# Kernel tuning notes

Measured on AMD Instinct MI355X. Metric: run time of the kernel, lower is better.

The kernel has to match this reference:

```python
import jax, jax.numpy as jnp
import numpy as np

ATTEN = 32  # window half-size; window = 2*ATTEN + 1


def _pos_enc(seq_len, hidden_size):
    # Faithful to original: pos_enc[pos, j] = pos / 10000**(2*(j//2)/hidden_size)
    # then sin on even columns, cos on odd columns. Shape [seq_len, seq_len].
    pos = jnp.arange(seq_len, dtype=jnp.float32)[:, None]
    j = jnp.arange(seq_len)
    inv = jnp.power(jnp.float32(10000.0), (2.0 * (j // 2).astype(jnp.float32)) / hidden_size)
    angle = pos / inv[None, :]
    return jnp.where((j % 2 == 0)[None, :], jnp.sin(angle), jnp.cos(angle))


def setup_inputs() -> dict:
    key = jax.random.key(0)
    ks = jax.random.split(key, 8)
    B, S, D_in, H, D_out = 4, 2048, 2048, 128, 2
    sd_in = 1.0 / np.sqrt(D_in)
    sd_h = 1.0 / np.sqrt(H)
    return {
        "x": jax.random.normal(ks[0], (B, S, D_in), dtype=jnp.float32),
        "W1": jax.random.normal(ks[1], (D_in, H), dtype=jnp.float32) * sd_in,
        "b1": jnp.zeros((H,), dtype=jnp.float32),
        "Wq": jax.random.normal(ks[2], (H, H), dtype=jnp.float32) * sd_h,
        "Wk": jax.random.normal(ks[3], (H, H), dtype=jnp.float32) * sd_h,
        "Wv": jax.random.normal(ks[4], (H, H), dtype=jnp.float32) * sd_h,
        "Wo": jax.random.normal(ks[5], (H, D_out), dtype=jnp.float32) * sd_h,
        "bo": jnp.zeros((D_out,), dtype=jnp.float32),
    }


def reference(x, W1, b1, Wq, Wk, Wv, Wo, bo):
    B, S, _ = x.shape
    H = W1.shape[1]
    scale = jnp.float32(np.sqrt(float(H)))

    x = x + _pos_enc(S, H)[None]                      # [B,S,D_in] (D_in == S)
    h = jax.nn.relu(x @ W1 + b1)                      # [B,S,H]

    # Replicate pad + roll(+wraparound) + stack + slice via a gather.
    # x_nei[b,i,j] = padded[b, (i + 2a - j) mod (S+2a)], j in [0, 2a].
    a = ATTEN
    L = S + 2 * a
    padded = jnp.pad(h, ((0, 0), (a, a), (0, 0)))     # [B,L,H]
    idx = (jnp.arange(S)[:, None] + 2 * a - jnp.arange(2 * a + 1)[None, :]) % L
    x_nei = padded[:, idx, :]                         # [B,S,2a+1,H]

    q = h @ Wq                                        # [B,S,H]
    k = x_nei @ Wk                                    # [B,S,2a+1,H]
    v = x_nei @ Wv                                    # [B,S,2a+1,H]

    scores = jnp.einsum('bid,bijd->bij', q, k) / scale
    atten_weights = jax.nn.softmax(scores, axis=-1)   # [B,S,2a+1]
    context = jnp.einsum('bij,bijd->bid', atten_weights, v) / scale  # extra /sqrt(H), faithful to source
    output = context @ Wo + bo                        # [B,S,D_out]
    return output, atten_weights
```

## Files before the change

### kernel.cpp

```cpp
#include <hip/hip_runtime.h>
#include <hip/hip_bf16.h>

typedef __attribute__((ext_vector_type(8))) _Float16 half8;
typedef __attribute__((ext_vector_type(4))) _Float16 half4;
typedef __attribute__((ext_vector_type(4))) float f32x4;

#define MFMAH(a,b,c) __builtin_amdgcn_mfma_f32_16x16x32_f16(a,b,c,0,0,0)

#define LOG2_10K_64 0.2076205059304595f
#define INV2PI 0.15915494309189535f

__global__ __launch_bounds__(256) void k_prep(const float* __restrict__ W1,
                                              const float* __restrict__ Wq,
                                              const float* __restrict__ Wk,
                                              const float* __restrict__ Wv,
                                              _Float16* __restrict__ W1t,
                                              _Float16* __restrict__ Wqkvt) {
  const int bid = blockIdx.x, tid = threadIdx.x;
  if (bid < 64) {
    __shared__ float Tl[64][65];
    const int kt0 = (bid >> 1) * 64, nt0 = (bid & 1) * 64;
    const int row = tid >> 2, c0 = (tid & 3) * 16;
#pragma unroll
    for (int e = 0; e < 16; e += 4) {
      float4 f = *(const float4*)(W1 + (size_t)(kt0 + row) * 128 + nt0 + c0 + e);
      Tl[row][c0 + e] = f.x; Tl[row][c0 + e + 1] = f.y;
      Tl[row][c0 + e + 2] = f.z; Tl[row][c0 + e + 3] = f.w;
    }
    __syncthreads();
    const int nrow = tid >> 2, kc0 = (tid & 3) * 16;
    _Float16* wp = W1t + (size_t)(nt0 + nrow) * 2048 + kt0 + kc0;
#pragma unroll
    for (int e = 0; e < 16; ++e) wp[e] = (_Float16)Tl[kc0 + e][nrow];
  } else {
    int r = (bid - 64) * 256 + tid;
    if (r < 3 * 16384) {
      int m = r >> 14, e = r & 16383;
      int n = e >> 7, k = e & 127;
      const float* W = (m == 0) ? Wq : (m == 1) ? Wk : Wv;
      Wqkvt[r] = (_Float16)W[k * 128 + n];
    }
  }
}

__global__ __launch_bounds__(512) void k_fused(const float* __restrict__ x,
                                               const _Float16* __restrict__ W1t,
                                               const _Float16* __restrict__ Wqkv,
                                               const float* __restrict__ b1,
                                               _Float16* __restrict__ Qg,
                                               _Float16* __restrict__ Kg,
                                               _Float16* __restrict__ Vg) {
  __shared__ _Float16 As[2][16][136];
  const int tid = threadIdx.x;
  const int lane = tid & 63, wv = tid >> 6;
  const int fr = lane & 15, kg8 = (lane >> 4) * 8;
  const int i0 = blockIdx.x * 16;
  const int arow = tid >> 5, akc = (tid & 31) * 4;
  const float sf = (float)((i0 + arow) & 2047);
  const float* xrow = x + (size_t)(i0 + arow) * 2048 + akc;
  const _Float16* wrow = W1t + (size_t)(wv * 16 + fr) * 2048 + kg8;

  auto loadB = [&](int s, half8* b) {
    const _Float16* p = wrow + s * 128;
#pragma unroll
    for (int kk = 0; kk < 4; ++kk) b[kk] = *(const half8*)(p + kk * 32);
  };
  auto stageA = [&](int buf, int s, float4 xa) {
    const int kb = s * 128 + akc;
    float c0 = exp2f((float)(kb >> 1) * -LOG2_10K_64) * INV2PI;
    float c1 = exp2f((float)((kb >> 1) + 1) * -LOG2_10K_64) * INV2PI;
    float r0 = __builtin_fmaf(sf, c0, -rintf(sf * c0));
    float r1 = __builtin_fmaf(sf, c1, -rintf(sf * c1));
    half4 av;
    av[0] = (_Float16)(xa.x + __builtin_amdgcn_sinf(r0));
    av[1] = (_Float16)(xa.y + __builtin_amdgcn_cosf(r0));
    av[2] = (_Float16)(xa.z + __builtin_amdgcn_sinf(r1));
    av[3] = (_Float16)(xa.w + __builtin_amdgcn_cosf(r1));
    *(half4*)&As[buf][arow][akc] = av;
  };

  float4 xaA = *(const float4*)(xrow);
  float4 xaB = *(const float4*)(xrow + 128);
  half8 bcur[4], bnxt[4];
  loadB(0, bcur);
  stageA(0, 0, xaA);
  __syncthreads();

  f32x4 acc = {};
#pragma unroll 1
  for (int i = 0; i < 7; ++i) {
    const int s = 2 * i;
    xaA = *(const float4*)(xrow + (s + 2) * 128);
    loadB(s + 1, bnxt);
#pragma unroll
    for (int kk = 0; kk < 4; ++kk) {
      half8 a = *(const half8*)&As[0][fr][kk * 32 + kg8];
      acc = MFMAH(a, bcur[kk], acc);
    }
    stageA(1, s + 1, xaB);
    __syncthreads();
    xaB = *(const float4*)(xrow + (s + 3) * 128);
    loadB(s + 2, bcur);
#pragma unroll
    for (int kk = 0; kk < 4; ++kk) {
      half8 a = *(const half8*)&As[1][fr][kk * 32 + kg8];
      acc = MFMAH(a, bnxt[kk], acc);
    }
    stageA(0, s + 2, xaA);
    __syncthreads();
  }
  loadB(15, bnxt);
#pragma unroll
  for (int kk = 0; kk < 4; ++kk) {
    half8 a = *(const half8*)&As[0][fr][kk * 32 + kg8];
    acc = MFMAH(a, bcur[kk], acc);
  }
  stageA(1, 15, xaB);
  __syncthreads();
#pragma unroll
  for (int kk = 0; kk < 4; ++kk) {
    half8 a = *(const half8*)&As[1][fr][kk * 32 + kg8];
    acc = MFMAH(a, bnxt[kk], acc);
  }
  __syncthreads();

  _Float16 (*Hs)[136] = As[0];
  {
    const int col = wv * 16 + fr;
    const float bv = b1[col];
#pragma unroll
    for (int r = 0; r < 4; ++r) {
      float v = acc[r] + bv;
      v = v > 0.f ? v : 0.f;
      Hs[(lane >> 4) * 4 + r][col] = (_Float16)v;
    }
  }
  __syncthreads();
  const _Float16* wqrow = Wqkv + (size_t)(wv * 16 + fr) * 128 + kg8;
#pragma unroll 1
  for (int m = 0; m < 3; ++m) {
    f32x4 a2 = {};
#pragma unroll
    for (int kk = 0; kk < 4; ++kk) {
      half8 a = *(const half8*)&Hs[fr][kk * 32 + kg8];
      half8 b = *(const half8*)(wqrow + m * 16384 + kk * 32);
      a2 = MFMAH(a, b, a2);
    }
    _Float16* dst = (m == 0) ? Qg : (m == 1) ? Kg : Vg;
#pragma unroll
    for (int r = 0; r < 4; ++r)
      dst[(size_t)(i0 + (lane >> 4) * 4 + r) * 128 + wv * 16 + fr] = (_Float16)a2[r];
  }
}

__global__ __launch_bounds__(256) void k_attn(const _Float16* __restrict__ Qg,
                                              const _Float16* __restrict__ Kg,
                                              const _Float16* __restrict__ Vg,
                                              const float* __restrict__ Wo,
                                              const float* __restrict__ bo,
                                              float* __restrict__ outp,
                                              float* __restrict__ attwg) {
  __shared__ _Float16 Qs[16][136];
  __shared__ _Float16 Ks[80][136];
  __shared__ _Float16 Vs[96][136];
  __shared__ _Float16 Ps[16][104];
  __shared__ float sc[16][84];
  __shared__ float aw[16 * 65];
  __shared__ float wol[128][2];
  __shared__ float proj[4][16][2];
  const int tid = threadIdx.x;
  const int lane = tid & 63, wv = tid >> 6;
  const int b = blockIdx.x >> 7;
  const int i0 = (blockIdx.x & 127) << 4;
  const int rowbase = b * 2048 + i0;
  const float invscale = 0.08838834764831845f;

  {
    const int row = tid >> 4, d8 = (tid & 15) * 8;
    *(half8*)&Qs[row][d8] = *(const half8*)(Qg + (size_t)(rowbase + row) * 128 + d8);
  }
#pragma unroll
  for (int it = 0; it < 5; ++it) {
    const int idx = it * 256 + tid;
    const int lr = idx >> 4, d8 = (idx & 15) * 8;
    const int j = i0 - 32 + lr;
    half8 kv = {0, 0, 0, 0, 0, 0, 0, 0};
    if (j >= 0 && j < 2048)
      kv = *(const half8*)(Kg + (size_t)(b * 2048 + j) * 128 + d8);
    *(half8*)&Ks[lr][d8] = kv;
  }
#pragma unroll
  for (int it = 0; it < 6; ++it) {
    const int idx = it * 256 + tid;
    const int lr = idx >> 4, d8 = (idx & 15) * 8;
    const int j = i0 - 32 + lr;
    half8 vv = {0, 0, 0, 0, 0, 0, 0, 0};
    if (lr < 80 && j >= 0 && j < 2048)
      vv = *(const half8*)(Vg + (size_t)(b * 2048 + j) * 128 + d8);
    *(half8*)&Vs[lr][d8] = vv;
  }
  wol[tid >> 1][tid & 1] = Wo[tid];
  __syncthreads();

  const int fr = lane & 15, kg8 = (lane >> 4) * 8;
  {
    const int nct = (wv == 0) ? 2 : 1;
    for (int p = 0; p < nct; ++p) {
      const int ct = (p == 0) ? wv : 4;
      f32x4 acc = {};
#pragma unroll
      for (int kk = 0; kk < 4; ++kk) {
        half8 a  = *(const half8*)&Qs[fr][kk * 32 + kg8];
        half8 bb = *(const half8*)&Ks[ct * 16 + fr][kk * 32 + kg8];
        acc = MFMAH(a, bb, acc);
      }
#pragma unroll
      for (int r = 0; r < 4; ++r)
        sc[(lane >> 4) * 4 + r][ct * 16 + fr] = acc[r] * invscale;
    }
  }
  __syncthreads();

#pragma unroll 1
  for (int rr = 0; rr < 4; ++rr) {
    const int r = wv * 4 + rr;
    const int c0 = lane;
    const bool ib0 = (c0 >= r);
    const bool ib1 = (lane <= r);
    float a0 = ib0 ? sc[r][c0] : -1e30f;
    float a1 = ib1 ? sc[r][64 + lane] : -1e30f;
    float mx = fmaxf(a0, a1);
#pragma unroll
    for (int o = 1; o < 64; o <<= 1) mx = fmaxf(mx, __shfl_xor(mx, o));
    float e0 = ib0 ? __expf(a0 - mx) : 0.f;
    float e1 = ib1 ? __expf(a1 - mx) : 0.f;
    float sm = e0 + e1;
#pragma unroll
    for (int o = 1; o < 64; o <<= 1) sm += __shfl_xor(sm, o);
    const float inv = 1.0f / sm;
    const float w0 = e0 * inv, w1 = e1 * inv;
    if (ib0) aw[r * 65 + (r + 64 - c0)] = w0;
    if (ib1) aw[r * 65 + (r - lane)] = w1;
    Ps[r][c0] = (_Float16)w0;
    if (lane < 32) Ps[r][64 + lane] = (_Float16)((lane < 16) ? w1 : 0.f);
  }
  __syncthreads();

  for (int i = tid; i < 1040; i += 256)
    attwg[(size_t)rowbase * 65 + i] = aw[i];

  f32x4 c2[2] = {};
#pragma unroll
  for (int kk = 0; kk < 3; ++kk) {
    half8 a = *(const half8*)&Ps[fr][kk * 32 + kg8];
#pragma unroll
    for (int dt2 = 0; dt2 < 2; ++dt2) {
      const int d = (2 * wv + dt2) * 16 + fr;
      half8 bb;
#pragma unroll
      for (int e = 0; e < 8; ++e) bb[e] = Vs[kk * 32 + kg8 + e][d];
      c2[dt2] = MFMAH(a, bb, c2[dt2]);
    }
  }
#pragma unroll
  for (int r = 0; r < 4; ++r) {
    float p0 = 0.f, p1 = 0.f;
#pragma unroll
    for (int dt2 = 0; dt2 < 2; ++dt2) {
      const int d = (2 * wv + dt2) * 16 + fr;
      p0 += c2[dt2][r] * wol[d][0];
      p1 += c2[dt2][r] * wol[d][1];
    }
    p0 += __shfl_xor(p0, 1); p0 += __shfl_xor(p0, 2);
    p0 += __shfl_xor(p0, 4); p0 += __shfl_xor(p0, 8);
    p1 += __shfl_xor(p1, 1); p1 += __shfl_xor(p1, 2);
    p1 += __shfl_xor(p1, 4); p1 += __shfl_xor(p1, 8);
    if (fr == 0) {
      const int q = (lane >> 4) * 4 + r;
      proj[wv][q][0] = p0;
      proj[wv][q][1] = p1;
    }
  }
  __syncthreads();
  if (tid < 16) {
    float s0 = proj[0][tid][0] + proj[1][tid][0] + proj[2][tid][0] + proj[3][tid][0];
    float s1 = proj[0][tid][1] + proj[1][tid][1] + proj[2][tid][1] + proj[3][tid][1];
    outp[((size_t)rowbase + tid) * 2 + 0] = s0 * invscale + bo[0];
    outp[((size_t)rowbase + tid) * 2 + 1] = s1 * invscale + bo[1];
  }
}

extern "C" void kernel_launch(void* const* d_in, const int* in_sizes, int n_in,
                              void* d_out, int out_size, void* d_ws, size_t ws_size,
                              hipStream_t stream) {
  const float* x  = (const float*)d_in[0];
  const float* W1 = (const float*)d_in[1];
  const float* b1 = (const float*)d_in[2];
  const float* Wq = (const float*)d_in[3];
  const float* Wk = (const float*)d_in[4];
  const float* Wv = (const float*)d_in[5];
  const float* Wo = (const float*)d_in[6];
  const float* bo = (const float*)d_in[7];
  float* out  = (float*)d_out;
  float* attw = out + 16384;

  _Float16* W1t  = (_Float16*)d_ws;
  _Float16* Wqkv = W1t + 262144;
  _Float16* Qg   = Wqkv + 49152;
  _Float16* Kg   = Qg + 1048576;
  _Float16* Vg   = Kg + 1048576;

  k_prep<<<256, 256, 0, stream>>>(W1, Wq, Wk, Wv, W1t, Wqkv);
  k_fused<<<512, 512, 0, stream>>>(x, W1t, Wqkv, b1, Qg, Kg, Vg);
  k_attn<<<512, 256, 0, stream>>>(Qg, Kg, Vg, Wo, bo, out, attw);
}
```

Before: 58.06 us.

## Precompute positional encoding table and split W1 GEMM over K across waves

Moves the sin/cos positional-encoding computation out of the GEMM mainloop into a precomputed fp16 table built in the prep kernel (1024 extra blocks). The fused kernel now drops LDS staging and per-step barriers: each wave loads x and the PE table directly into registers and computes a 16x64 tile over one quarter of K. The partial sums are then reduced through shared memory before bias and ReLU. This removes the transcendental work and synchronisation from the inner loop, at the cost of an extra 8 MB table write and read each call and an added cross-wave reduction.

```diff
diff --git a/kernel.cpp b/kernel.cpp
--- a/kernel.cpp
+++ b/kernel.cpp
@@ -15,7 +15,8 @@
                                               const float* __restrict__ Wk,
                                               const float* __restrict__ Wv,
                                               _Float16* __restrict__ W1t,
-                                              _Float16* __restrict__ Wqkvt) {
+                                              _Float16* __restrict__ Wqkvt,
+                                              _Float16* __restrict__ Pe) {
   const int bid = blockIdx.x, tid = threadIdx.x;
   if (bid < 64) {
     __shared__ float Tl[64][65];
@@ -32,7 +33,7 @@
     _Float16* wp = W1t + (size_t)(nt0 + nrow) * 2048 + kt0 + kc0;
 #pragma unroll
     for (int e = 0; e < 16; ++e) wp[e] = (_Float16)Tl[kc0 + e][nrow];
-  } else {
+  } else if (bid < 256) {
     int r = (bid - 64) * 256 + tid;
     if (r < 3 * 16384) {
       int m = r >> 14, e = r & 16383;
@@ -40,102 +41,96 @@
       const float* W = (m == 0) ? Wq : (m == 1) ? Wk : Wv;
       Wqkvt[r] = (_Float16)W[k * 128 + n];
     }
+  } else {
+    const int g = (bid - 256) * 256 + tid;
+    const int s = g >> 7;
+    const int j0 = (g & 127) * 16;
+    const float sf = (float)s;
+    half8 o0, o1;
+#pragma unroll
+    for (int p = 0; p < 8; ++p) {
+      const int jh = (j0 >> 1) + p;
+      float c = exp2f((float)jh * -LOG2_10K_64) * INV2PI;
+      float r = __builtin_fmaf(sf, c, -rintf(sf * c));
+      _Float16 sn = (_Float16)__builtin_amdgcn_sinf(r);
+      _Float16 cs = (_Float16)__builtin_amdgcn_cosf(r);
+      if (p < 4) { o0[2 * p] = sn; o0[2 * p + 1] = cs; }
+      else       { o1[2 * (p - 4)] = sn; o1[2 * (p - 4) + 1] = cs; }
+    }
+    _Float16* dst = Pe + (size_t)s * 2048 + j0;
+    *(half8*)dst = o0;
+    *(half8*)(dst + 8) = o1;
   }
 }
 
 __global__ __launch_bounds__(512) void k_fused(const float* __restrict__ x,
                                                const _Float16* __restrict__ W1t,
+                                               const _Float16* __restrict__ Pe,
                                                const _Float16* __restrict__ Wqkv,
                                                const float* __restrict__ b1,
                                                _Float16* __restrict__ Qg,
                                                _Float16* __restrict__ Kg,
                                                _Float16* __restrict__ Vg) {
-  __shared__ _Float16 As[2][16][136];
+  __shared__ float Hp[4][16][132];
+  __shared__ _Float16 Hs[16][136];
   const int tid = threadIdx.x;
   const int lane = tid & 63, wv = tid >> 6;
+  const int kg = wv >> 1, cg = wv & 1;
   const int fr = lane & 15, kg8 = (lane >> 4) * 8;
   const int i0 = blockIdx.x * 16;
-  const int arow = tid >> 5, akc = (tid & 31) * 4;
-  const float sf = (float)((i0 + arow) & 2047);
-  const float* xrow = x + (size_t)(i0 + arow) * 2048 + akc;
-  const _Float16* wrow = W1t + (size_t)(wv * 16 + fr) * 2048 + kg8;
-
-  auto loadB = [&](int s, half8* b) {
-    const _Float16* p = wrow + s * 128;
-#pragma unroll
-    for (int kk = 0; kk < 4; ++kk) b[kk] = *(const half8*)(p + kk * 32);
-  };
-  auto stageA = [&](int buf, int s, float4 xa) {
-    const int kb = s * 128 + akc;
-    float c0 = exp2f((float)(kb >> 1) * -LOG2_10K_64) * INV2PI;
-    float c1 = exp2f((float)((kb >> 1) + 1) * -LOG2_10K_64) * INV2PI;
-    float r0 = __builtin_fmaf(sf, c0, -rintf(sf * c0));
-    float r1 = __builtin_fmaf(sf, c1, -rintf(sf * c1));
-    half4 av;
-    av[0] = (_Float16)(xa.x + __builtin_amdgcn_sinf(r0));
-    av[1] = (_Float16)(xa.y + __builtin_amdgcn_cosf(r0));
-    av[2] = (_Float16)(xa.z + __builtin_amdgcn_sinf(r1));
-    av[3] = (_Float16)(xa.w + __builtin_amdgcn_cosf(r1));
-    *(half4*)&As[buf][arow][akc] = av;
-  };
-
-  float4 xaA = *(const float4*)(xrow);
-  float4 xaB = *(const float4*)(xrow + 128);
-  half8 bcur[4], bnxt[4];
-  loadB(0, bcur);
-  stageA(0, 0, xaA);
-  __syncthreads();
-
-  f32x4 acc = {};
+
+  const float*    xs  = x   + (size_t)(i0 + fr) * 2048 + kg * 512 + kg8;
+  const _Float16* pes = Pe  + (size_t)((i0 + fr) & 2047) * 2048 + kg * 512 + kg8;
+  const _Float16* ws  = W1t + (size_t)(cg * 64 + fr) * 2048 + kg * 512 + kg8;
+
+  f32x4 acc[4] = {};
 #pragma unroll 1
-  for (int i = 0; i < 7; ++i) {
-    const int s = 2 * i;
-    xaA = *(const float4*)(xrow + (s + 2) * 128);
-    loadB(s + 1, bnxt);
+  for (int s = 0; s < 4; ++s) {
 #pragma unroll
     for (int kk = 0; kk < 4; ++kk) {
-      half8 a = *(const half8*)&As[0][fr][kk * 32 + kg8];
-      acc = MFMAH(a, bcur[kk], acc);
-    }
-    stageA(1, s + 1, xaB);
-    __syncthreads();
-    xaB = *(const float4*)(xrow + (s + 3) * 128);
-    loadB(s + 2, bcur);
-#pragma unroll
-    for (int kk = 0; kk < 4; ++kk) {
-      half8 a = *(const half8*)&As[1][fr][kk * 32 + kg8];
-      acc = MFMAH(a, bnxt[kk], acc);
-    }
-    stageA(0, s + 2, xaA);
-    __syncthreads();
-  }
-  loadB(15, bnxt);
-#pragma unroll
-  for (int kk = 0; kk < 4; ++kk) {
-    half8 a = *(const half8*)&As[0][fr][kk * 32 + kg8];
-    acc = MFMAH(a, bcur[kk], acc);
-  }
-  stageA(1, 15, xaB);
-  __syncthreads();
-#pragma unroll
-  for (int kk = 0; kk < 4; ++kk) {
-    half8 a = *(const half8*)&As[1][fr][kk * 32 + kg8];
-    acc = MFMAH(a, bnxt[kk], acc);
-  }
-  __syncthreads();
-
-  _Float16 (*Hs)[136] = As[0];
+      f32x4 x0 = *(const f32x4*)(xs + kk * 32);
+      f32x4 x1 = *(const f32x4*)(xs + kk * 32 + 4);
+      half8 pe = *(const half8*)(pes + kk * 32);
+      half8 af;
+#pragma unroll
+      for (int e = 0; e < 4; ++e) af[e] = (_Float16)(x0[e] + (float)pe[e]);
+#pragma unroll
+      for (int e = 0; e < 4; ++e) af[4 + e] = (_Float16)(x1[e] + (float)pe[4 + e]);
+#pragma unroll
+      for (int ct = 0; ct < 4; ++ct) {
+        half8 b = *(const half8*)(ws + ct * 32768 + kk * 32);
+        acc[ct] = MFMAH(af, b, acc[ct]);
+      }
+    }
+    xs += 128; pes += 128; ws += 128;
+  }
+
+#pragma unroll
+  for (int ct = 0; ct < 4; ++ct)
+#pragma unroll
+    for (int r = 0; r < 4; ++r)
+      Hp[kg][(lane >> 4) * 4 + r][cg * 64 + ct * 16 + fr] = acc[ct][r];
+  __syncthreads();
+
   {
-    const int col = wv * 16 + fr;
-    const float bv = b1[col];
-#pragma unroll
-    for (int r = 0; r < 4; ++r) {
-      float v = acc[r] + bv;
-      v = v > 0.f ? v : 0.f;
-      Hs[(lane >> 4) * 4 + r][col] = (_Float16)v;
-    }
-  }
-  __syncthreads();
+    const int row = tid >> 5, col = (tid & 31) * 4;
+    f32x4 v = *(const f32x4*)&Hp[0][row][col];
+#pragma unroll
+    for (int k2 = 1; k2 < 4; ++k2) {
+      f32x4 p = *(const f32x4*)&Hp[k2][row][col];
+#pragma unroll
+      for (int e = 0; e < 4; ++e) v[e] += p[e];
+    }
+    half4 hv;
+#pragma unroll
+    for (int e = 0; e < 4; ++e) {
+      float t = v[e] + b1[col + e];
+      hv[e] = (_Float16)(t > 0.f ? t : 0.f);
+    }
+    *(half4*)&Hs[row][col] = hv;
+  }
+  __syncthreads();
+
   const _Float16* wqrow = Wqkv + (size_t)(wv * 16 + fr) * 128 + kg8;
 #pragma unroll 1
   for (int m = 0; m < 3; ++m) {
@@ -306,11 +301,12 @@
 
   _Float16* W1t  = (_Float16*)d_ws;
   _Float16* Wqkv = W1t + 262144;
-  _Float16* Qg   = Wqkv + 49152;
+  _Float16* Pe   = Wqkv + 49152;
+  _Float16* Qg   = Pe + 4194304;
   _Float16* Kg   = Qg + 1048576;
   _Float16* Vg   = Kg + 1048576;
 
-  k_prep<<<256, 256, 0, stream>>>(W1, Wq, Wk, Wv, W1t, Wqkv);
-  k_fused<<<512, 512, 0, stream>>>(x, W1t, Wqkv, b1, Qg, Kg, Vg);
+  k_prep<<<1280, 256, 0, stream>>>(W1, Wq, Wk, Wv, W1t, Wqkv, Pe);
+  k_fused<<<512, 512, 0, stream>>>(x, W1t, Pe, Wqkv, b1, Qg, Kg, Vg);
   k_attn<<<512, 256, 0, stream>>>(Qg, Kg, Vg, Wo, bo, out, attw);
 }
```

New measurement: 78.74 us. 1.36x slower.
